# Performance work log

Hardware: AMD Instinct MI355X
Metric: run time of the kernel (lower is better)

## Reference

```python
import jax, jax.numpy as jnp
import numpy as np

NUM_POINTS = 100
K = 10
NEG = 0.2  # LeakyReLU slope


def knn_idx(x, k):
    # x: [B, C, N] -> idx [B, N, k] of k nearest neighbors (incl. self)
    xx = jnp.sum(x * x, axis=1)                      # [B, N]
    inner = jnp.einsum('bcn,bcm->bnm', x, x)         # [B, N, N]
    dist = 2.0 * inner - xx[:, :, None] - xx[:, None, :]  # -(squared dist)
    return jax.lax.top_k(dist, k)[1]                 # [B, N, k]


def get_graph_feature(x, k):
    # x: [B, C, N] -> [B, 2C, N, k] with (neighbor - center, center)
    B, C, N = x.shape
    idx = knn_idx(x, k)                              # [B, N, k]
    xt = jnp.transpose(x, (0, 2, 1))                 # [B, N, C]
    feat = xt[jnp.arange(B)[:, None, None], idx]     # [B, N, k, C]
    center = xt[:, :, None, :]                       # [B, N, 1, C]
    out = jnp.concatenate([feat - center, jnp.broadcast_to(center, feat.shape)], axis=-1)
    return jnp.transpose(out, (0, 3, 1, 2))          # [B, 2C, N, k]


def conv1d_bn(x, W, s, t):
    # 1x1 conv (no bias) + eval-mode BN folded to affine + LeakyReLU. x: [B,C,N]
    y = jnp.einsum('oc,bcn->bon', W, x)
    return jax.nn.leaky_relu(y * s[:, None] + t[:, None], NEG)


def conv2d_bn(x, W, s, t):
    # 1x1 conv (no bias) + BN affine + LeakyReLU. x: [B,C,N,k]
    y = jnp.einsum('oc,bcnk->bonk', W, x)
    return jax.nn.leaky_relu(y * s[:, None, None] + t[:, None, None], NEG)


def setup_inputs() -> dict:
    key = jax.random.key(0)
    ks = jax.random.split(key, 40)
    B, S = 1024, 3000
    cin = S // NUM_POINTS  # 30

    def w(k, o, c):
        return jax.random.normal(k, (o, c), jnp.float32) * 0.05

    def sc(k, c):
        return jax.random.uniform(k, (c,), jnp.float32, 0.5, 1.5)

    def sh(k, c):
        return jax.random.normal(k, (c,), jnp.float32) * 0.05

    obs = jax.random.normal(ks[0], (B, S), jnp.float32)
    inp = {'obs': obs,
           'W0': w(ks[1], 32, cin), 'W1': w(ks[2], 32, 64), 'W2': w(ks[3], 32, 32),
           'W3': w(ks[4], 32, 64), 'W4': w(ks[5], 32, 32), 'W5': w(ks[6], 32, 64),
           'W6': w(ks[7], 512, 96), 'W7': w(ks[8], 128, 608), 'W8': w(ks[9], 32, 128),
           'W9': w(ks[10], 1, 32)}
    dims = [32, 32, 32, 32, 32, 32, 512, 128, 32]
    for i, d in enumerate(dims):
        inp[f's{i}'] = sc(ks[11 + i], d)
        inp[f't{i}'] = sh(ks[20 + i], d)
    return inp


def reference(obs, W0, W1, W2, W3, W4, W5, W6, W7, W8, W9,
              s0, s1, s2, s3, s4, s5, s6, s7, s8,
              t0, t1, t2, t3, t4, t5, t6, t7, t8):
    cin = obs.shape[-1] // NUM_POINTS
    x = obs.reshape(-1, NUM_POINTS, cin).transpose(0, 2, 1)  # [B, C_in, N]
    B, _, N = x.shape

    x = conv1d_bn(x, W0, s0, t0)                 # [B, 32, N]

    f = get_graph_feature(x, K)                  # [B, 64, N, K]
    f = conv2d_bn(f, W1, s1, t1)
    f = conv2d_bn(f, W2, s2, t2)
    x1 = jnp.max(f, axis=-1)                     # [B, 32, N]

    f = get_graph_feature(x1, K)
    f = conv2d_bn(f, W3, s3, t3)
    f = conv2d_bn(f, W4, s4, t4)
    x2 = jnp.max(f, axis=-1)                     # [B, 32, N]

    f = get_graph_feature(x2, K)
    f = conv2d_bn(f, W5, s5, t5)
    x3 = jnp.max(f, axis=-1)                     # [B, 32, N]

    xc = jnp.concatenate([x1, x2, x3], axis=1)   # [B, 96, N]
    xe = conv1d_bn(xc, W6, s6, t6)               # [B, 512, N]
    g = jnp.max(xe, axis=-1, keepdims=True)      # [B, 512, 1]
    g = jnp.broadcast_to(g, (B, 512, N))
    h = jnp.concatenate([g, x1, x2, x3], axis=1)  # [B, 608, N]
    h = conv1d_bn(h, W7, s7, t7)                 # [B, 128, N]
    h = conv1d_bn(h, W8, s8, t8)                 # [B, 32, N]
    # dropout is identity in eval mode
    out = jnp.einsum('oc,bcn->bon', W9, h)       # [B, 1, N]
    return jnp.squeeze(out, axis=1)              # [B, N]
```

## Files before the change

kernel.cpp:

```cpp
#include <hip/hip_runtime.h>

#define NPT 100
#define KK 10

typedef __attribute__((ext_vector_type(8))) short short8;
typedef __attribute__((ext_vector_type(4))) float float4v;

__device__ __forceinline__ float leaky(float v){ return fmaxf(v, 0.2f*v); }
__device__ __forceinline__ unsigned short bf16r(float x){
  unsigned u = __float_as_uint(x);
  return (unsigned short)((u + 0x7FFFu + ((u>>16)&1u)) >> 16);
}
__device__ __forceinline__ float bf2f(unsigned short h){ return __uint_as_float(((unsigned)h)<<16); }

#define WV(w) (1024*(w))
#define W7G_OFF 9216
#define W6B_OFF   299008
#define W796B_OFF 593920
#define W8B_OFF   667648

struct PrepP {
  const float* W[9];
  const float* s[9];
  float* ws;
};

__global__ __launch_bounds__(256) void prep_kernel(PrepP p){
  int gid = blockIdx.x*256 + threadIdx.x;
  int gs = gridDim.x*256;
  float* ws = p.ws;
  unsigned short* w6b  = (unsigned short*)((char*)ws + W6B_OFF);
  unsigned short* w796 = (unsigned short*)((char*)ws + W796B_OFF);
  unsigned short* w8b  = (unsigned short*)((char*)ws + W8B_OFF);
  for(int i = gid; i < 9216; i += gs){
    int w = i >> 10, r = i & 1023, o = r >> 5, c = r & 31;
    float v = 0.f;
    switch(w){
      case 0: v = (c < 30) ? p.s[0][o]*p.W[0][o*30 + c] : 0.f; break;
      case 1: v = p.s[1][o]*p.W[1][o*64 + c]; break;
      case 2: v = p.s[1][o]*(p.W[1][o*64 + 32 + c] - p.W[1][o*64 + c]); break;
      case 3: v = p.s[2][o]*p.W[2][o*32 + c]; break;
      case 4: v = p.s[3][o]*p.W[3][o*64 + c]; break;
      case 5: v = p.s[3][o]*(p.W[3][o*64 + 32 + c] - p.W[3][o*64 + c]); break;
      case 6: v = p.s[4][o]*p.W[4][o*32 + c]; break;
      case 7: v = p.s[5][o]*p.W[5][o*64 + c]; break;
      case 8: v = p.s[5][o]*(p.W[5][o*64 + 32 + c] - p.W[5][o*64 + c]); break;
    }
    ws[i] = v;
  }
  for(int i = gid; i < 65536; i += gs){
    int o = i >> 9, c = i & 511;
    ws[W7G_OFF + i] = p.s[7][o]*p.W[7][o*608 + c];
  }
  for(int i = gid; i < 147456; i += gs){
    int o = i/288, cc = i - o*288, kb = cc >> 5, k = cc & 31;
    int sc = (kb % 3)*32 + k;
    float w = p.s[6][o]*p.W[6][o*96 + sc];
    unsigned short h = bf16r(w);
    w6b[i] = (kb < 6) ? h : bf16r(w - bf2f(h));
  }
  for(int i = gid; i < 36864; i += gs){
    int o = i/288, cc = i - o*288, kb = cc >> 5, k = cc & 31;
    int sc = 512 + (kb % 3)*32 + k;
    float w = p.s[7][o]*p.W[7][o*608 + sc];
    unsigned short h = bf16r(w);
    w796[i] = (kb < 6) ? h : bf16r(w - bf2f(h));
  }
  for(int i = gid; i < 12288; i += gs){
    int o = i/384, cc = i - o*384, kb = cc >> 5, k = cc & 31;
    int sc = (kb & 3)*32 + k;
    float w = p.s[8][o]*p.W[8][o*128 + sc];
    unsigned short h = bf16r(w);
    w8b[i] = (kb < 8) ? h : bf16r(w - bf2f(h));
  }
}

__device__ __forceinline__ void load32(const float* src, float* xr){
  #pragma unroll
  for(int q = 0; q < 8; ++q){
    float4v v = *(const float4v*)&src[q*4];
    xr[q*4+0] = v.x; xr[q*4+1] = v.y; xr[q*4+2] = v.z; xr[q*4+3] = v.w;
  }
}
__device__ __forceinline__ float dot32(const float* wrow, const float* xr){
  float a0 = 0.f, a1 = 0.f, a2 = 0.f, a3 = 0.f;
  #pragma unroll
  for(int q = 0; q < 8; ++q){
    float4v w = *(const float4v*)&wrow[q*4];
    a0 = fmaf(w.x, xr[q*4+0], a0);
    a1 = fmaf(w.y, xr[q*4+1], a1);
    a2 = fmaf(w.z, xr[q*4+2], a2);
    a3 = fmaf(w.w, xr[q*4+3], a3);
  }
  return (a0+a1)+(a2+a3);
}
__device__ __forceinline__ void buildB(const float* src, short8* bh, short8* bl){
  float4v v0 = *(const float4v*)&src[0];
  float4v v1 = *(const float4v*)&src[4];
  float xv[8] = {v0.x, v0.y, v0.z, v0.w, v1.x, v1.y, v1.z, v1.w};
  short8 h, l;
  #pragma unroll
  for(int j = 0; j < 8; ++j){
    unsigned short hh = bf16r(xv[j]);
    h[j] = (short)hh;
    l[j] = (short)bf16r(xv[j] - bf2f(hh));
  }
  *bh = h; *bl = l;
}

__device__ __forceinline__ void conv2_chunk2(int n, int k0, int ob,
    const unsigned char* IDXB, const float* PREG, const float* qt,
    const float* WST, float* acc){
  float e0[32], e1[32];
  #pragma unroll
  for(int kk = 0; kk < 2; ++kk){
    float* e = kk ? e1 : e0;
    int j = IDXB[n*KK + k0 + kk];
    #pragma unroll
    for(int q = 0; q < 8; ++q){
      float4v pv = *(const float4v*)&PREG[j*36 + q*4];
      e[q*4+0] = leaky(pv.x + qt[q*4+0]);
      e[q*4+1] = leaky(pv.y + qt[q*4+1]);
      e[q*4+2] = leaky(pv.z + qt[q*4+2]);
      e[q*4+3] = leaky(pv.w + qt[q*4+3]);
    }
  }
  #pragma unroll
  for(int o = 0; o < 8; ++o){
    float d0a = 0.f, d0b = 0.f, d1a = 0.f, d1b = 0.f;
    #pragma unroll
    for(int q = 0; q < 8; ++q){
      float4v w = *(const float4v*)&WST[(ob + o)*32 + q*4];
      d0a = fmaf(w.x, e0[q*4+0], d0a); d0b = fmaf(w.y, e0[q*4+1], d0b);
      d0a = fmaf(w.z, e0[q*4+2], d0a); d0b = fmaf(w.w, e0[q*4+3], d0b);
      d1a = fmaf(w.x, e1[q*4+0], d1a); d1b = fmaf(w.y, e1[q*4+1], d1b);
      d1a = fmaf(w.z, e1[q*4+2], d1a); d1b = fmaf(w.w, e1[q*4+3], d1b);
    }
    acc[o] = fmaxf(acc[o], fmaxf(d0a + d0b, d1a + d1b));
  }
}

struct MainP {
  const float* obs;
  const float* W9;
  const float* t[9];
  const float* ws;
  float* out;
};

__global__ __launch_bounds__(256, 2) void dgcnn(MainP p){
  const int b = blockIdx.x;
  const int tid = threadIdx.x;
  const int lane = tid & 63, wv = tid >> 6;
  const int quad = lane >> 4, l15 = lane & 15;

  __shared__ __align__(16) float XBIG[10000];
  __shared__ __align__(16) float PREG[3600];
  __shared__ __align__(16) float WST[2048];
  __shared__ __align__(16) float XX[100];
  __shared__ __align__(16) float TMP[32];
  __shared__ unsigned char IDXB[1000];

  const float* ws = p.ws;
  const unsigned short* w6b  = (const unsigned short*)((const char*)ws + W6B_OFF);
  const unsigned short* w796 = (const unsigned short*)((const char*)ws + W796B_OFF);
  const unsigned short* w8b  = (const unsigned short*)((const char*)ws + W8B_OFF);

  for(int i = tid; i < 3600; i += 256){
    int n = i/36, c = i - n*36;
    PREG[i] = (c < 30) ? p.obs[(size_t)b*3000 + n*30 + c] : 0.f;
  }
  for(int i = tid; i < 1024; i += 256) WST[i] = ws[WV(0) + i];
  __syncthreads();

  if(tid < NPT){
    float xr[32]; load32(&PREG[tid*36], xr);
    #pragma unroll
    for(int ob = 0; ob < 8; ++ob){
      float4v y;
      #pragma unroll
      for(int oi = 0; oi < 4; ++oi){
        int o = ob*4 + oi;
        y[oi] = leaky(dot32(&WST[o*32], xr) + p.t[0][o]);
      }
      *(float4v*)&XBIG[tid*100 + 64 + ob*4] = y;
    }
  }
  __syncthreads();

  const int XINs[3]  = {64, 0, 32};
  const int QOFFs[3] = {32, 64, 0};
  const int OUTs[3]  = {0, 32, 64};
  const int WPI[3]   = {1, 4, 7};

  for(int L = 0; L < 3; ++L){
    const int XIN = XINs[L], OUT = OUTs[L], QOFF = QOFFs[L];
    for(int i = tid; i < 1024; i += 256){
      WST[i]        = ws[WV(WPI[L])   + i];
      WST[1024 + i] = ws[WV(WPI[L]+1) + i];
    }
    __syncthreads();
    if(tid < NPT){
      float xr[32]; load32(&XBIG[tid*100 + XIN], xr);
      float a = 0.f;
      #pragma unroll
      for(int c = 0; c < 32; ++c) a = fmaf(xr[c], xr[c], a);
      XX[tid] = a;
    }
    __syncthreads();
    if(tid < 128){
      if(tid < NPT){
        const int n = tid;
        float xr[32]; load32(&XBIG[n*100 + XIN], xr);
        const float xxn = XX[n];
        float bv[KK]; int bj[KK];
        #pragma unroll
        for(int k = 0; k < KK; ++k){ bv[k] = -3.4e38f; bj[k] = 0; }
        #pragma unroll 1
        for(int m = 0; m < NPT; ++m){
          const float* xm = &XBIG[m*100 + XIN];
          float a0 = 0.f, a1 = 0.f, a2 = 0.f, a3 = 0.f;
          #pragma unroll
          for(int q = 0; q < 8; ++q){
            float4v v = *(const float4v*)&xm[q*4];
            a0 = fmaf(xr[q*4+0], v.x, a0);
            a1 = fmaf(xr[q*4+1], v.y, a1);
            a2 = fmaf(xr[q*4+2], v.z, a2);
            a3 = fmaf(xr[q*4+3], v.w, a3);
          }
          float d = 2.0f*((a0+a1)+(a2+a3)) - xxn - XX[m];
          if(d > bv[KK-1]){
            float cv = d; int ci = m;
            #pragma unroll
            for(int jj = 0; jj < KK; ++jj){
              bool sw = cv > bv[jj];
              float tv = bv[jj]; int ti = bj[jj];
              bv[jj] = sw ? cv : tv; bj[jj] = sw ? ci : ti;
              cv = sw ? tv : cv;    ci = sw ? ti : ci;
            }
          }
        }
        #pragma unroll
        for(int k = 0; k < KK; ++k) IDXB[n*KK + k] = (unsigned char)bj[k];
      }
    } else {
      int j = tid - 128;
      if(j < NPT){
        float xr[32]; load32(&XBIG[j*100 + XIN], xr);
        #pragma unroll 1
        for(int o = 0; o < 32; ++o) PREG[j*36 + o] = dot32(&WST[o*32], xr);
        if(L < 2){
          #pragma unroll 1
          for(int o = 0; o < 32; ++o) XBIG[j*100 + QOFF + o] = dot32(&WST[1024 + o*32], xr);
        }
      }
    }
    __syncthreads();

    if(L < 2){
      int wci = (L == 0) ? 3 : 6;
      for(int i = tid; i < 1024; i += 256) WST[i] = ws[WV(wci) + i];
      if(tid < 32){
        WST[1024 + tid] = p.t[1 + 2*L][tid];
        WST[1056 + tid] = p.t[2 + 2*L][tid];
      }
      __syncthreads();
      for(int it = tid; it < 400; it += 256){
        int n = it % 100, oct = it / 100, ob = oct*8;
        float qt[32];
        #pragma unroll
        for(int q = 0; q < 8; ++q){
          float4v qv = *(const float4v*)&XBIG[n*100 + QOFF + q*4];
          float4v tv = *(const float4v*)&WST[1024 + q*4];
          qt[q*4+0] = qv.x + tv.x; qt[q*4+1] = qv.y + tv.y;
          qt[q*4+2] = qv.z + tv.z; qt[q*4+3] = qv.w + tv.w;
        }
        float acc[8];
        #pragma unroll
        for(int o = 0; o < 8; ++o) acc[o] = -3.4e38f;
        conv2_chunk2(n, 0, ob, IDXB, PREG, qt, WST, acc);
        conv2_chunk2(n, 2, ob, IDXB, PREG, qt, WST, acc);
        conv2_chunk2(n, 4, ob, IDXB, PREG, qt, WST, acc);
        conv2_chunk2(n, 6, ob, IDXB, PREG, qt, WST, acc);
        conv2_chunk2(n, 8, ob, IDXB, PREG, qt, WST, acc);
        #pragma unroll
        for(int oh = 0; oh < 2; ++oh){
          float4v y;
          #pragma unroll
          for(int oi = 0; oi < 4; ++oi){
            int o = ob + oh*4 + oi;
            y[oi] = leaky(acc[oh*4 + oi] + WST[1056 + o]);
          }
          *(float4v*)&XBIG[n*100 + OUT + ob + oh*4] = y;
        }
      }
      __syncthreads();
    } else {
      if(tid < NPT){
        float xr[32]; load32(&XBIG[tid*100 + XIN], xr);
        float pm[32];
        #pragma unroll
        for(int o = 0; o < 32; ++o) pm[o] = -3.4e38f;
        #pragma unroll 1
        for(int k = 0; k < KK; ++k){
          int j = IDXB[tid*KK + k];
          #pragma unroll
          for(int q = 0; q < 8; ++q){
            float4v pv = *(const float4v*)&PREG[j*36 + q*4];
            pm[q*4+0] = fmaxf(pm[q*4+0], pv.x);
            pm[q*4+1] = fmaxf(pm[q*4+1], pv.y);
            pm[q*4+2] = fmaxf(pm[q*4+2], pv.z);
            pm[q*4+3] = fmaxf(pm[q*4+3], pv.w);
          }
        }
        #pragma unroll 1
        for(int o = 0; o < 32; ++o){
          float qv = dot32(&WST[1024 + o*32], xr);
          XBIG[tid*100 + OUT + o] = leaky(pm[o] + qv + p.t[5][o]);
        }
      }
      __syncthreads();
    }
  }

  {
    float4v gmax[8];
    #pragma unroll
    for(int i = 0; i < 8; ++i){ gmax[i][0] = -3.4e38f; gmax[i][1] = -3.4e38f; gmax[i][2] = -3.4e38f; gmax[i][3] = -3.4e38f; }
    #pragma unroll 1
    for(int nt = 0; nt < 7; ++nt){
      int row = nt*16 + l15; if(row > 99) row = 99;
      short8 Bh[3], Bl[3];
      #pragma unroll
      for(int g = 0; g < 3; ++g) buildB(&XBIG[row*100 + g*32 + quad*8], &Bh[g], &Bl[g]);
      #pragma unroll 1
      for(int mt = 0; mt < 8; ++mt){
        int orow = (wv*8 + mt)*16 + l15;
        const unsigned short* ar = w6b + orow*288 + quad*8;
        float4v d = {0.f, 0.f, 0.f, 0.f};
        #pragma unroll
        for(int kb = 0; kb < 9; ++kb){
          short8 a = *(const short8*)(ar + kb*32);
          short8 bb = (kb < 3) ? Bh[kb] : ((kb < 6) ? Bl[kb-3] : Bh[kb-6]);
          d = __builtin_amdgcn_mfma_f32_16x16x32_bf16(a, bb, d, 0, 0, 0);
        }
        #pragma unroll
        for(int r = 0; r < 4; ++r) gmax[mt][r] = fmaxf(gmax[mt][r], d[r]);
      }
    }
    #pragma unroll 1
    for(int mt = 0; mt < 8; ++mt){
      float4v m = gmax[mt];
      #pragma unroll
      for(int bit = 1; bit < 16; bit <<= 1){
        m[0] = fmaxf(m[0], __shfl_xor(m[0], bit, 64));
        m[1] = fmaxf(m[1], __shfl_xor(m[1], bit, 64));
        m[2] = fmaxf(m[2], __shfl_xor(m[2], bit, 64));
        m[3] = fmaxf(m[3], __shfl_xor(m[3], bit, 64));
      }
      if(l15 == 0){
        #pragma unroll
        for(int r = 0; r < 4; ++r){
          int o = (wv*8 + mt)*16 + quad*4 + r;
          WST[o] = leaky(m[r] + p.t[6][o]);
        }
      }
    }
  }
  __syncthreads();

  if(tid < 128){
    const float* wr = &ws[W7G_OFF + tid*512];
    float a0 = 0.f, a1 = 0.f, a2 = 0.f, a3 = 0.f;
    #pragma unroll 4
    for(int c4 = 0; c4 < 128; ++c4){
      float4v w = *(const float4v*)&wr[c4*4];
      float4v g = *(const float4v*)&WST[c4*4];
      a0 = fmaf(w.x, g.x, a0); a1 = fmaf(w.y, g.y, a1);
      a2 = fmaf(w.z, g.z, a2); a3 = fmaf(w.w, g.w, a3);
    }
    WST[512 + tid] = (a0+a1)+(a2+a3);
  }
  __syncthreads();

  float* H2 = PREG;
  #pragma unroll 1
  for(int nc = 0; nc < 7; ++nc){
    int n0 = nc*16;
    int row = n0 + l15; if(row > 99) row = 99;
    short8 Bh[3], Bl[3];
    #pragma unroll
    for(int g = 0; g < 3; ++g) buildB(&XBIG[row*100 + g*32 + quad*8], &Bh[g], &Bl[g]);
    #pragma unroll 1
    for(int mm = 0; mm < 2; ++mm){
      int Mt = wv*2 + mm;
      const unsigned short* ar = w796 + (Mt*16 + l15)*288 + quad*8;
      float4v d = {0.f, 0.f, 0.f, 0.f};
      #pragma unroll
      for(int kb = 0; kb < 9; ++kb){
        short8 a = *(const short8*)(ar + kb*32);
        short8 bb = (kb < 3) ? Bh[kb] : ((kb < 6) ? Bl[kb-3] : Bh[kb-6]);
        d = __builtin_amdgcn_mfma_f32_16x16x32_bf16(a, bb, d, 0, 0, 0);
      }
      float4v y;
      #pragma unroll
      for(int r = 0; r < 4; ++r){
        int ch = Mt*16 + quad*4 + r;
        y[r] = leaky(d[r] + WST[512 + ch] + p.t[7][ch]);
      }
      *(float4v*)&H2[l15*132 + Mt*16 + quad*4] = y;
    }
    __syncthreads();
    if(wv < 2){
      short8 Ch[4], Cl[4];
      #pragma unroll
      for(int g = 0; g < 4; ++g) buildB(&H2[l15*132 + g*32 + quad*8], &Ch[g], &Cl[g]);
      const unsigned short* ar = w8b + (wv*16 + l15)*384 + quad*8;
      float4v d = {0.f, 0.f, 0.f, 0.f};
      #pragma unroll
      for(int kb = 0; kb < 12; ++kb){
        short8 a = *(const short8*)(ar + kb*32);
        short8 bb = (kb < 4) ? Ch[kb] : ((kb < 8) ? Cl[kb-4] : Ch[kb-8]);
        d = __builtin_amdgcn_mfma_f32_16x16x32_bf16(a, bb, d, 0, 0, 0);
      }
      float partial = 0.f;
      #pragma unroll
      for(int r = 0; r < 4; ++r){
        int o = wv*16 + quad*4 + r;
        float h3 = leaky(d[r] + p.t[8][o]);
        partial = fmaf(p.W9[o], h3, partial);
      }
      partial += __shfl_xor(partial, 16, 64);
      partial += __shfl_xor(partial, 32, 64);
      if(lane < 16) TMP[wv*16 + lane] = partial;
    }
    __syncthreads();
    if(tid < 16 && (n0 + tid) < NPT)
      p.out[(size_t)b*NPT + n0 + tid] = TMP[tid] + TMP[16 + tid];
    __syncthreads();
  }
}

extern "C" void kernel_launch(void* const* d_in, const int* in_sizes, int n_in,
                              void* d_out, int out_size, void* d_ws, size_t ws_size,
                              hipStream_t stream) {
  (void)n_in; (void)out_size; (void)ws_size;
  PrepP pp;
  for(int i = 0; i < 9; ++i) pp.W[i] = (const float*)d_in[1 + i];
  for(int i = 0; i < 9; ++i) pp.s[i] = (const float*)d_in[11 + 2*i];
  pp.ws = (float*)d_ws;
  prep_kernel<<<256, 256, 0, stream>>>(pp);

  MainP mp;
  mp.obs = (const float*)d_in[0];
  mp.W9  = (const float*)d_in[10];
  for(int i = 0; i < 9; ++i) mp.t[i] = (const float*)d_in[12 + 2*i];
  mp.ws  = (const float*)d_ws;
  mp.out = (float*)d_out;
  const int B = in_sizes[0] / 3000;
  dgcnn<<<B, 256, 0, stream>>>(mp);
}
```

Before: 716.8 us.

## Double block to 512 threads, split kNN search, swizzle LDS layout

```diff
diff --git a/kernel.cpp b/kernel.cpp
--- a/kernel.cpp
+++ b/kernel.cpp
@@ -75,10 +75,13 @@
   }
 }
 
-__device__ __forceinline__ void load32(const float* src, float* xr){
+__device__ __forceinline__ int xcq(int n, int q){ return n*24 + (q ^ (n & 7)); }
+__device__ __forceinline__ int pq(int j, int q){ return j*8 + (q ^ (j & 7)); }
+
+__device__ __forceinline__ void loadxg(const float* XB, int row, int gq, float* xr){
   #pragma unroll
   for(int q = 0; q < 8; ++q){
-    float4v v = *(const float4v*)&src[q*4];
+    float4v v = *(const float4v*)&XB[xcq(row, gq + q) << 2];
     xr[q*4+0] = v.x; xr[q*4+1] = v.y; xr[q*4+2] = v.z; xr[q*4+3] = v.w;
   }
 }
@@ -93,6 +96,20 @@
     a3 = fmaf(w.w, xr[q*4+3], a3);
   }
   return (a0+a1)+(a2+a3);
+}
+__device__ __forceinline__ void buildB2(const float* XB, int row, int g, int quad,
+                                        short8* bh, short8* bl){
+  float4v v0 = *(const float4v*)&XB[xcq(row, g*8 + quad*2)     << 2];
+  float4v v1 = *(const float4v*)&XB[xcq(row, g*8 + quad*2 + 1) << 2];
+  float xv[8] = {v0.x, v0.y, v0.z, v0.w, v1.x, v1.y, v1.z, v1.w};
+  short8 h, l;
+  #pragma unroll
+  for(int j = 0; j < 8; ++j){
+    unsigned short hh = bf16r(xv[j]);
+    h[j] = (short)hh;
+    l[j] = (short)bf16r(xv[j] - bf2f(hh));
+  }
+  *bh = h; *bl = l;
 }
 __device__ __forceinline__ void buildB(const float* src, short8* bh, short8* bl){
   float4v v0 = *(const float4v*)&src[0];
@@ -108,38 +125,6 @@
   *bh = h; *bl = l;
 }
 
-__device__ __forceinline__ void conv2_chunk2(int n, int k0, int ob,
-    const unsigned char* IDXB, const float* PREG, const float* qt,
-    const float* WST, float* acc){
-  float e0[32], e1[32];
-  #pragma unroll
-  for(int kk = 0; kk < 2; ++kk){
-    float* e = kk ? e1 : e0;
-    int j = IDXB[n*KK + k0 + kk];
-    #pragma unroll
-    for(int q = 0; q < 8; ++q){
-      float4v pv = *(const float4v*)&PREG[j*36 + q*4];
-      e[q*4+0] = leaky(pv.x + qt[q*4+0]);
-      e[q*4+1] = leaky(pv.y + qt[q*4+1]);
-      e[q*4+2] = leaky(pv.z + qt[q*4+2]);
-      e[q*4+3] = leaky(pv.w + qt[q*4+3]);
-    }
-  }
-  #pragma unroll
-  for(int o = 0; o < 8; ++o){
-    float d0a = 0.f, d0b = 0.f, d1a = 0.f, d1b = 0.f;
-    #pragma unroll
-    for(int q = 0; q < 8; ++q){
-      float4v w = *(const float4v*)&WST[(ob + o)*32 + q*4];
-      d0a = fmaf(w.x, e0[q*4+0], d0a); d0b = fmaf(w.y, e0[q*4+1], d0b);
-      d0a = fmaf(w.z, e0[q*4+2], d0a); d0b = fmaf(w.w, e0[q*4+3], d0b);
-      d1a = fmaf(w.x, e1[q*4+0], d1a); d1b = fmaf(w.y, e1[q*4+1], d1b);
-      d1a = fmaf(w.z, e1[q*4+2], d1a); d1b = fmaf(w.w, e1[q*4+3], d1b);
-    }
-    acc[o] = fmaxf(acc[o], fmaxf(d0a + d0b, d1a + d1b));
-  }
-}
-
 struct MainP {
   const float* obs;
   const float* W9;
@@ -148,15 +133,15 @@
   float* out;
 };
 
-__global__ __launch_bounds__(256, 2) void dgcnn(MainP p){
+__global__ __launch_bounds__(512, 4) void dgcnn(MainP p){
   const int b = blockIdx.x;
   const int tid = threadIdx.x;
   const int lane = tid & 63, wv = tid >> 6;
   const int quad = lane >> 4, l15 = lane & 15;
 
-  __shared__ __align__(16) float XBIG[10000];
-  __shared__ __align__(16) float PREG[3600];
-  __shared__ __align__(16) float WST[2048];
+  __shared__ __align__(16) float XBIG[9600];
+  __shared__ __align__(16) float PREG[3200];
+  __shared__ __align__(16) float WST[3072];
   __shared__ __align__(16) float XX[100];
   __shared__ __align__(16) float TMP[32];
   __shared__ unsigned char IDXB[1000];
@@ -166,63 +151,63 @@
   const unsigned short* w796 = (const unsigned short*)((const char*)ws + W796B_OFF);
   const unsigned short* w8b  = (const unsigned short*)((const char*)ws + W8B_OFF);
 
-  for(int i = tid; i < 3600; i += 256){
-    int n = i/36, c = i - n*36;
-    PREG[i] = (c < 30) ? p.obs[(size_t)b*3000 + n*30 + c] : 0.f;
-  }
-  for(int i = tid; i < 1024; i += 256) WST[i] = ws[WV(0) + i];
+  for(int i = tid; i < 3200; i += 512){
+    int n = i >> 5, c = i & 31;
+    float v = (c < 30) ? p.obs[(size_t)b*3000 + n*30 + c] : 0.f;
+    XBIG[(xcq(n, c >> 2) << 2) | (c & 3)] = v;
+  }
+  for(int i = tid; i < 1024; i += 512) WST[i] = ws[WV(0) + i];
   __syncthreads();
 
-  if(tid < NPT){
-    float xr[32]; load32(&PREG[tid*36], xr);
-    #pragma unroll
-    for(int ob = 0; ob < 8; ++ob){
-      float4v y;
-      #pragma unroll
-      for(int oi = 0; oi < 4; ++oi){
-        int o = ob*4 + oi;
-        y[oi] = leaky(dot32(&WST[o*32], xr) + p.t[0][o]);
-      }
-      *(float4v*)&XBIG[tid*100 + 64 + ob*4] = y;
+  {
+    int oh = tid >> 7, n = tid & 127;
+    if(n < NPT){
+      float xr[32]; loadxg(XBIG, n, 0, xr);
+      float o8[8];
+      #pragma unroll
+      for(int oi = 0; oi < 8; ++oi){
+        int o = oh*8 + oi;
+        o8[oi] = leaky(dot32(&WST[o*32], xr) + p.t[0][o]);
+      }
+      *(float4v*)&XBIG[xcq(n, 16 + oh*2)     << 2] = *(float4v*)&o8[0];
+      *(float4v*)&XBIG[xcq(n, 16 + oh*2 + 1) << 2] = *(float4v*)&o8[4];
     }
   }
   __syncthreads();
 
-  const int XINs[3]  = {64, 0, 32};
-  const int QOFFs[3] = {32, 64, 0};
-  const int OUTs[3]  = {0, 32, 64};
-  const int WPI[3]   = {1, 4, 7};
+  const int XINq[3] = {16, 0, 8};
+  const int QOFq[3] = {8, 16, 0};
+  const int OUTq[3] = {0, 8, 16};
+  const int OUTc[3] = {0, 32, 64};
+  const int WPI[3]  = {1, 4, 7};
 
   for(int L = 0; L < 3; ++L){
-    const int XIN = XINs[L], OUT = OUTs[L], QOFF = QOFFs[L];
-    for(int i = tid; i < 1024; i += 256){
-      WST[i]        = ws[WV(WPI[L])   + i];
-      WST[1024 + i] = ws[WV(WPI[L]+1) + i];
-    }
+    for(int i = tid; i < 2048; i += 512) WST[i] = ws[WV(WPI[L]) + i];
     __syncthreads();
     if(tid < NPT){
-      float xr[32]; load32(&XBIG[tid*100 + XIN], xr);
+      float xr[32]; loadxg(XBIG, tid, XINq[L], xr);
       float a = 0.f;
       #pragma unroll
       for(int c = 0; c < 32; ++c) a = fmaf(xr[c], xr[c], a);
       XX[tid] = a;
     }
     __syncthreads();
-    if(tid < 128){
-      if(tid < NPT){
-        const int n = tid;
-        float xr[32]; load32(&XBIG[n*100 + XIN], xr);
+
+    if(tid < 256){
+      int n = tid & 127, h = tid >> 7;
+      if(n < NPT){
+        float xr[32]; loadxg(XBIG, n, XINq[L], xr);
         const float xxn = XX[n];
         float bv[KK]; int bj[KK];
         #pragma unroll
         for(int k = 0; k < KK; ++k){ bv[k] = -3.4e38f; bj[k] = 0; }
+        const int m0 = h*50;
         #pragma unroll 1
-        for(int m = 0; m < NPT; ++m){
-          const float* xm = &XBIG[m*100 + XIN];
+        for(int m = m0; m < m0 + 50; ++m){
           float a0 = 0.f, a1 = 0.f, a2 = 0.f, a3 = 0.f;
           #pragma unroll
           for(int q = 0; q < 8; ++q){
-            float4v v = *(const float4v*)&xm[q*4];
+            float4v v = *(const float4v*)&XBIG[xcq(m, XINq[L] + q) << 2];
             a0 = fmaf(xr[q*4+0], v.x, a0);
             a1 = fmaf(xr[q*4+1], v.y, a1);
             a2 = fmaf(xr[q*4+2], v.z, a2);
@@ -240,103 +225,158 @@
             }
           }
         }
-        #pragma unroll
-        for(int k = 0; k < KK; ++k) IDXB[n*KK + k] = (unsigned char)bj[k];
+        float* rowraw = &XBIG[n*96 + OUTc[L]];
+        unsigned char* rowb = (unsigned char*)rowraw;
+        #pragma unroll
+        for(int k = 0; k < KK; ++k){
+          int slot = (h*10 + k + n) % 20;
+          rowraw[slot] = bv[k];
+          rowb[80 + slot] = (unsigned char)bj[k];
+        }
+      }
+    } else if(tid < 384){
+      int j = tid - 256;
+      if(j < NPT){
+        float xr[32]; loadxg(XBIG, j, XINq[L], xr);
+        #pragma unroll 1
+        for(int og = 0; og < 4; ++og){
+          float t[8];
+          #pragma unroll
+          for(int oi = 0; oi < 8; ++oi) t[oi] = dot32(&WST[(og*8 + oi)*32], xr);
+          *(float4v*)&PREG[pq(j, og*2)     << 2] = *(float4v*)&t[0];
+          *(float4v*)&PREG[pq(j, og*2 + 1) << 2] = *(float4v*)&t[4];
+        }
       }
     } else {
-      int j = tid - 128;
-      if(j < NPT){
-        float xr[32]; load32(&XBIG[j*100 + XIN], xr);
+      if(L < 2){
+        int wci = (L == 0) ? 3 : 6;
+        for(int i = tid - 384; i < 1024; i += 128) WST[2048 + i] = ws[WV(wci) + i];
+        int n = tid - 384;
+        if(n < NPT){
+          const float* ta = p.t[1 + 2*L];
+          float xr[32]; loadxg(XBIG, n, XINq[L], xr);
+          #pragma unroll 1
+          for(int og = 0; og < 4; ++og){
+            float t[8];
+            #pragma unroll
+            for(int oi = 0; oi < 8; ++oi)
+              t[oi] = dot32(&WST[1024 + (og*8 + oi)*32], xr) + ta[og*8 + oi];
+            *(float4v*)&XBIG[xcq(n, QOFq[L] + og*2)     << 2] = *(float4v*)&t[0];
+            *(float4v*)&XBIG[xcq(n, QOFq[L] + og*2 + 1) << 2] = *(float4v*)&t[4];
+          }
+        }
+      }
+    }
+    __syncthreads();
+
+    if(tid < NPT){
+      const int n = tid;
+      const float* rowraw = &XBIG[n*96 + OUTc[L]];
+      const unsigned char* rowb = (const unsigned char*)rowraw;
+      int ia = 0, ib = 0;
+      #pragma unroll
+      for(int k = 0; k < KK; ++k){
+        bool canA = ia < 10, canB = ib < 10;
+        float va = canA ? rowraw[(ia + n) % 20]      : -3.4e38f;
+        float vb = canB ? rowraw[(10 + ib + n) % 20] : -3.4e38f;
+        bool takeb = canB && (!canA || (vb > va));
+        int slot = takeb ? ((10 + ib + n) % 20) : ((ia + n) % 20);
+        IDXB[n*KK + k] = rowb[80 + slot];
+        ia += takeb ? 0 : 1;
+        ib += takeb ? 1 : 0;
+      }
+    }
+    __syncthreads();
+
+    if(L < 2){
+      int n = tid & 127, oct = tid >> 7, ob = oct*8;
+      if(n < NPT){
+        const float* tb = p.t[2 + 2*L];
+        float qp[32]; loadxg(XBIG, n, QOFq[L], qp);
+        float acc[8];
+        #pragma unroll
+        for(int o = 0; o < 8; ++o) acc[o] = -3.4e38f;
         #pragma unroll 1
-        for(int o = 0; o < 32; ++o) PREG[j*36 + o] = dot32(&WST[o*32], xr);
-        if(L < 2){
-          #pragma unroll 1
-          for(int o = 0; o < 32; ++o) XBIG[j*100 + QOFF + o] = dot32(&WST[1024 + o*32], xr);
-        }
-      }
-    }
-    __syncthreads();
-
-    if(L < 2){
-      int wci = (L == 0) ? 3 : 6;
-      for(int i = tid; i < 1024; i += 256) WST[i] = ws[WV(wci) + i];
-      if(tid < 32){
-        WST[1024 + tid] = p.t[1 + 2*L][tid];
-        WST[1056 + tid] = p.t[2 + 2*L][tid];
-      }
-      __syncthreads();
-      for(int it = tid; it < 400; it += 256){
-        int n = it % 100, oct = it / 100, ob = oct*8;
-        float qt[32];
-        #pragma unroll
-        for(int q = 0; q < 8; ++q){
-          float4v qv = *(const float4v*)&XBIG[n*100 + QOFF + q*4];
-          float4v tv = *(const float4v*)&WST[1024 + q*4];
-          qt[q*4+0] = qv.x + tv.x; qt[q*4+1] = qv.y + tv.y;
-          qt[q*4+2] = qv.z + tv.z; qt[q*4+3] = qv.w + tv.w;
-        }
-        float acc[8];
-        #pragma unroll
-        for(int o = 0; o < 8; ++o) acc[o] = -3.4e38f;
-        conv2_chunk2(n, 0, ob, IDXB, PREG, qt, WST, acc);
-        conv2_chunk2(n, 2, ob, IDXB, PREG, qt, WST, acc);
-        conv2_chunk2(n, 4, ob, IDXB, PREG, qt, WST, acc);
-        conv2_chunk2(n, 6, ob, IDXB, PREG, qt, WST, acc);
-        conv2_chunk2(n, 8, ob, IDXB, PREG, qt, WST, acc);
-        #pragma unroll
-        for(int oh = 0; oh < 2; ++oh){
-          float4v y;
+        for(int k = 0; k < KK; ++k){
+          int j = (int)IDXB[n*KK + k];
+          float e[32];
           #pragma unroll
-          for(int oi = 0; oi < 4; ++oi){
-            int o = ob + oh*4 + oi;
-            y[oi] = leaky(acc[oh*4 + oi] + WST[1056 + o]);
-          }
-          *(float4v*)&XBIG[n*100 + OUT + ob + oh*4] = y;
-        }
-      }
-      __syncthreads();
+          for(int q = 0; q < 8; ++q){
+            float4v pv = *(const float4v*)&PREG[pq(j, q) << 2];
+            e[q*4+0] = leaky(pv.x + qp[q*4+0]);
+            e[q*4+1] = leaky(pv.y + qp[q*4+1]);
+            e[q*4+2] = leaky(pv.z + qp[q*4+2]);
+            e[q*4+3] = leaky(pv.w + qp[q*4+3]);
+          }
+          #pragma unroll
+          for(int oi = 0; oi < 8; ++oi){
+            float d0 = 0.f, d1 = 0.f;
+            #pragma unroll
+            for(int q = 0; q < 8; ++q){
+              float4v w = *(const float4v*)&WST[2048 + (ob + oi)*32 + q*4];
+              d0 = fmaf(w.x, e[q*4+0], d0); d1 = fmaf(w.y, e[q*4+1], d1);
+              d0 = fmaf(w.z, e[q*4+2], d0); d1 = fmaf(w.w, e[q*4+3], d1);
+            }
+            acc[oi] = fmaxf(acc[oi], d0 + d1);
+          }
+        }
+        float y[8];
+        #pragma unroll
+        for(int oi = 0; oi < 8; ++oi) y[oi] = leaky(acc[oi] + tb[ob + oi]);
+        *(float4v*)&XBIG[xcq(n, OUTq[L] + oct*2)     << 2] = *(float4v*)&y[0];
+        *(float4v*)&XBIG[xcq(n, OUTq[L] + oct*2 + 1) << 2] = *(float4v*)&y[4];
+      }
     } else {
       if(tid < NPT){
-        float xr[32]; load32(&XBIG[tid*100 + XIN], xr);
+        const int n = tid;
         float pm[32];
         #pragma unroll
         for(int o = 0; o < 32; ++o) pm[o] = -3.4e38f;
         #pragma unroll 1
         for(int k = 0; k < KK; ++k){
-          int j = IDXB[tid*KK + k];
+          int j = (int)IDXB[n*KK + k];
           #pragma unroll
           for(int q = 0; q < 8; ++q){
-            float4v pv = *(const float4v*)&PREG[j*36 + q*4];
+            float4v pv = *(const float4v*)&PREG[pq(j, q) << 2];
             pm[q*4+0] = fmaxf(pm[q*4+0], pv.x);
             pm[q*4+1] = fmaxf(pm[q*4+1], pv.y);
             pm[q*4+2] = fmaxf(pm[q*4+2], pv.z);
             pm[q*4+3] = fmaxf(pm[q*4+3], pv.w);
           }
         }
+        float xr[32]; loadxg(XBIG, n, XINq[L], xr);
+        const float* t5 = p.t[5];
         #pragma unroll 1
-        for(int o = 0; o < 32; ++o){
-          float qv = dot32(&WST[1024 + o*32], xr);
-          XBIG[tid*100 + OUT + o] = leaky(pm[o] + qv + p.t[5][o]);
-        }
-      }
-      __syncthreads();
-    }
+        for(int og = 0; og < 4; ++og){
+          float y[8];
+          #pragma unroll
+          for(int oi = 0; oi < 8; ++oi){
+            int o = og*8 + oi;
+            float qv = dot32(&WST[1024 + o*32], xr);
+            y[oi] = leaky(pm[o] + qv + t5[o]);
+          }
+          *(float4v*)&XBIG[xcq(n, OUTq[L] + og*2)     << 2] = *(float4v*)&y[0];
+          *(float4v*)&XBIG[xcq(n, OUTq[L] + og*2 + 1) << 2] = *(float4v*)&y[4];
+        }
+      }
+    }
+    __syncthreads();
   }
 
   {
-    float4v gmax[8];
+    float4v gmax[4];
     #pragma unroll
-    for(int i = 0; i < 8; ++i){ gmax[i][0] = -3.4e38f; gmax[i][1] = -3.4e38f; gmax[i][2] = -3.4e38f; gmax[i][3] = -3.4e38f; }
+    for(int i = 0; i < 4; ++i){ gmax[i][0]=-3.4e38f; gmax[i][1]=-3.4e38f; gmax[i][2]=-3.4e38f; gmax[i][3]=-3.4e38f; }
     #pragma unroll 1
     for(int nt = 0; nt < 7; ++nt){
       int row = nt*16 + l15; if(row > 99) row = 99;
       short8 Bh[3], Bl[3];
       #pragma unroll
-      for(int g = 0; g < 3; ++g) buildB(&XBIG[row*100 + g*32 + quad*8], &Bh[g], &Bl[g]);
+      for(int g = 0; g < 3; ++g) buildB2(XBIG, row, g, quad, &Bh[g], &Bl[g]);
       #pragma unroll 1
-      for(int mt = 0; mt < 8; ++mt){
-        int orow = (wv*8 + mt)*16 + l15;
-        const unsigned short* ar = w6b + orow*288 + quad*8;
+      for(int mtl = 0; mtl < 4; ++mtl){
+        int T = wv*4 + mtl;
+        const unsigned short* ar = w6b + (T*16 + l15)*288 + quad*8;
         float4v d = {0.f, 0.f, 0.f, 0.f};
         #pragma unroll
         for(int kb = 0; kb < 9; ++kb){
@@ -345,12 +385,12 @@
           d = __builtin_amdgcn_mfma_f32_16x16x32_bf16(a, bb, d, 0, 0, 0);
         }
         #pragma unroll
-        for(int r = 0; r < 4; ++r) gmax[mt][r] = fmaxf(gmax[mt][r], d[r]);
+        for(int r = 0; r < 4; ++r) gmax[mtl][r] = fmaxf(gmax[mtl][r], d[r]);
       }
     }
     #pragma unroll 1
-    for(int mt = 0; mt < 8; ++mt){
-      float4v m = gmax[mt];
+    for(int mtl = 0; mtl < 4; ++mtl){
+      float4v m = gmax[mtl];
       #pragma unroll
       for(int bit = 1; bit < 16; bit <<= 1){
         m[0] = fmaxf(m[0], __shfl_xor(m[0], bit, 64));
@@ -359,9 +399,10 @@
         m[3] = fmaxf(m[3], __shfl_xor(m[3], bit, 64));
       }
       if(l15 == 0){
+        int T = wv*4 + mtl;
         #pragma unroll
         for(int r = 0; r < 4; ++r){
-          int o = (wv*8 + mt)*16 + quad*4 + r;
+          int o = T*16 + quad*4 + r;
           WST[o] = leaky(m[r] + p.t[6][o]);
         }
       }
@@ -369,17 +410,22 @@
   }
   __syncthreads();
 
-  if(tid < 128){
-    const float* wr = &ws[W7G_OFF + tid*512];
+  {
+    int o = tid >> 2, qtr = tid & 3;
+    const float* wr = &ws[W7G_OFF + o*512 + qtr*128];
+    const float* gr = &WST[qtr*128];
     float a0 = 0.f, a1 = 0.f, a2 = 0.f, a3 = 0.f;
     #pragma unroll 4
-    for(int c4 = 0; c4 < 128; ++c4){
+    for(int c4 = 0; c4 < 32; ++c4){
       float4v w = *(const float4v*)&wr[c4*4];
-      float4v g = *(const float4v*)&WST[c4*4];
+      float4v g = *(const float4v*)&gr[c4*4];
       a0 = fmaf(w.x, g.x, a0); a1 = fmaf(w.y, g.y, a1);
       a2 = fmaf(w.z, g.z, a2); a3 = fmaf(w.w, g.w, a3);
     }
-    WST[512 + tid] = (a0+a1)+(a2+a3);
+    float a = (a0+a1)+(a2+a3);
+    a += __shfl_xor(a, 1, 64);
+    a += __shfl_xor(a, 2, 64);
+    if(qtr == 0) WST[512 + o] = a;
   }
   __syncthreads();
 
@@ -388,12 +434,11 @@
   for(int nc = 0; nc < 7; ++nc){
     int n0 = nc*16;
     int row = n0 + l15; if(row > 99) row = 99;
-    short8 Bh[3], Bl[3];
-    #pragma unroll
-    for(int g = 0; g < 3; ++g) buildB(&XBIG[row*100 + g*32 + quad*8], &Bh[g], &Bl[g]);
-    #pragma unroll 1
-    for(int mm = 0; mm < 2; ++mm){
-      int Mt = wv*2 + mm;
+    {
+      short8 Bh[3], Bl[3];
+      #pragma unroll
+      for(int g = 0; g < 3; ++g) buildB2(XBIG, row, g, quad, &Bh[g], &Bl[g]);
+      const int Mt = wv;
       const unsigned short* ar = w796 + (Mt*16 + l15)*288 + quad*8;
       float4v d = {0.f, 0.f, 0.f, 0.f};
       #pragma unroll
@@ -402,13 +447,13 @@
         short8 bb = (kb < 3) ? Bh[kb] : ((kb < 6) ? Bl[kb-3] : Bh[kb-6]);
         d = __builtin_amdgcn_mfma_f32_16x16x32_bf16(a, bb, d, 0, 0, 0);
       }
-      float4v y;
+      float y[4];
       #pragma unroll
       for(int r = 0; r < 4; ++r){
         int ch = Mt*16 + quad*4 + r;
         y[r] = leaky(d[r] + WST[512 + ch] + p.t[7][ch]);
       }
-      *(float4v*)&H2[l15*132 + Mt*16 + quad*4] = y;
+      *(float4v*)&H2[l15*132 + Mt*16 + quad*4] = *(float4v*)&y[0];
     }
     __syncthreads();
     if(wv < 2){
@@ -458,5 +503,5 @@
   mp.ws  = (const float*)d_ws;
   mp.out = (float*)d_out;
   const int B = in_sizes[0] / 3000;
-  dgcnn<<<B, 256, 0, stream>>>(mp);
-}
+  dgcnn<<<B, 512, 0, stream>>>(mp);
+}
```

Result: slower. 2.063 ms (+187.9%).
